# Optimization experiments

Measured on AMD Instinct MI355X. Metric: run time of the kernel, lower is better.

Reference implementation:

```python
import jax, jax.numpy as jnp
import numpy as np
from jax import lax

B, C_IN, H, W = 128, 3, 64, 64
HID = 128          # encoder hidden channels
D = 256            # embedding_dim
K = 1024           # codebook_size
COMMIT = 0.25      # commitment_cost


def conv(x, w, b, stride=2, pad=1):
    # x: NCHW, w: OIHW (torch Conv2d layout)
    y = lax.conv_general_dilated(x, w, (stride, stride), [(pad, pad), (pad, pad)],
                                 dimension_numbers=('NCHW', 'OIHW', 'NCHW'))
    return y + b[None, :, None, None]


def conv_t(x, w, b, stride=2, pad=1):
    # torch ConvTranspose2d: w is (in, out, kh, kw); equivalent to a conv with
    # lhs dilation = stride, flipped kernel, padding k-1-pad.
    k = w.shape[2]
    w_ = jnp.flip(w, (2, 3)).transpose(1, 0, 2, 3)  # -> (out, in, kh, kw)
    p = k - 1 - pad
    y = lax.conv_general_dilated(x, w_, (1, 1), [(p, p), (p, p)],
                                 lhs_dilation=(stride, stride),
                                 dimension_numbers=('NCHW', 'OIHW', 'NCHW'))
    return y + b[None, :, None, None]


def setup_inputs() -> dict:
    key = jax.random.key(0)
    ks = jax.random.split(key, 10)
    s = 0.05
    return {
        'x':        jax.random.normal(ks[0], (B, C_IN, H, W), jnp.float32),
        'enc_w1':   jax.random.normal(ks[1], (HID, C_IN, 4, 4), jnp.float32) * s,
        'enc_b1':   jnp.zeros((HID,), jnp.float32),
        'enc_w2':   jax.random.normal(ks[2], (D, HID, 4, 4), jnp.float32) * s,
        'enc_b2':   jnp.zeros((D,), jnp.float32),
        'dec_w1':   jax.random.normal(ks[3], (D, HID, 4, 4), jnp.float32) * s,   # ConvT: (in,out,kh,kw)
        'dec_b1':   jnp.zeros((HID,), jnp.float32),
        'dec_w2':   jax.random.normal(ks[4], (HID, C_IN, 4, 4), jnp.float32) * s,
        'dec_b2':   jnp.zeros((C_IN,), jnp.float32),
        'codebook': jax.random.normal(ks[5], (K, D), jnp.float32),  # embedding.weight.normal_()
    }


def vqvae_forward(x, enc_w1, enc_b1, enc_w2, enc_b2,
                  dec_w1, dec_b1, dec_w2, dec_b2, codebook):
    # ----- encoder -----
    h = jax.nn.relu(conv(x, enc_w1, enc_b1))          # (B, HID, 32, 32)
    e = conv(h, enc_w2, enc_b2)                        # (B, D, 16, 16)

    # ----- VectorQuantizerEMA.forward (eval mode, no mask) -----
    inputs = e.transpose(0, 2, 3, 1)                   # BCHW -> BHWC
    in_shape = inputs.shape
    flat = inputs.reshape(-1, D)                       # (N, D), N = B*16*16

    # squared L2 distances to every code: (N, K)
    dist = (jnp.sum(flat * flat, axis=1, keepdims=True)
            + jnp.sum(codebook * codebook, axis=1)
            - 2.0 * flat @ codebook.T)

    # max_one_hot(-distances) with straight-through gradients
    logits = -dist
    idx = jnp.argmax(logits, axis=-1)                  # (N,)
    oh = jax.nn.one_hot(idx, K, dtype=logits.dtype)
    flat_oh = oh + logits - lax.stop_gradient(logits)  # values == one-hot

    n_lat = in_shape[1] * in_shape[2]                  # H*W latents
    oh_encodings = flat_oh.reshape(in_shape[0], n_lat, K).transpose(0, 2, 1)  # (B, K, n)

    # quantize under no_grad (torch.no_grad block)
    quantized = lax.stop_gradient(flat_oh @ codebook).reshape(in_shape)

    e_latent_loss = jnp.mean((quantized - inputs) ** 2)
    loss = COMMIT * e_latent_loss

    # straight-through estimator
    quantized = inputs + lax.stop_gradient(quantized - inputs)

    avg_probs = jnp.mean(flat_oh, axis=0)
    perplexity = jnp.exp(-jnp.sum(avg_probs * jnp.log(avg_probs + 1e-10)))

    quantized_nchw = quantized.transpose(0, 3, 1, 2)   # BHWC -> BCHW

    # ----- decoder -----
    d1 = jax.nn.relu(conv_t(quantized_nchw, dec_w1, dec_b1))  # (B, HID, 32, 32)
    x_hat = conv_t(d1, dec_w2, dec_b2)                        # (B, 3, 64, 64)

    return x_hat, loss, perplexity, oh_encodings


def reference(x, enc_w1, enc_b1, enc_w2, enc_b2,
              dec_w1, dec_b1, dec_w2, dec_b2, codebook):
    return vqvae_forward(x, enc_w1, enc_b1, enc_w2, enc_b2,
                         dec_w1, dec_b1, dec_w2, dec_b2, codebook)
```

## Files before the change

kernel.cpp:

```cpp
#include <hip/hip_runtime.h>
#include <stdint.h>

#define NB   128
#define CIN  3
#define HID  128
#define DEM  256
#define KCB  1024
#define NLAT 32768

typedef __bf16 bf16x8 __attribute__((ext_vector_type(8)));
typedef _Float16 f16x8 __attribute__((ext_vector_type(8)));
typedef float  f32x4  __attribute__((ext_vector_type(4)));

__device__ inline unsigned short f2bf(float f) {
    unsigned u = __builtin_bit_cast(unsigned, f);
    u = (u + 0x7fff + ((u >> 16) & 1)) >> 16;
    return (unsigned short)u;
}

__global__ __launch_bounds__(256) void k_conv1(const float* __restrict__ x,
        const float* __restrict__ w, const float* __restrict__ bias,
        unsigned short* __restrict__ hA) {
    __shared__ float sx[3][66][66];
    const int b = blockIdx.y;
    const int ocg = blockIdx.x;
    const int oc0 = ocg * 16;
    const int tid = threadIdx.x;
    for (int i = tid; i < 3 * 66 * 66; i += 256) ((float*)sx)[i] = 0.f;
    __syncthreads();
    const float* xb = x + (size_t)b * (3 * 64 * 64);
    for (int i = tid; i < 3 * 64 * 64; i += 256) {
        int ic = i >> 12; int rem = i & 4095; int y = rem >> 6; int xx = rem & 63;
        sx[ic][y + 1][xx + 1] = xb[i];
    }
    __syncthreads();
    for (int j = 0; j < 4; ++j) {
        int pos = tid + j * 256;
        int oy = pos >> 5, ox = pos & 31;
        float acc[16];
        #pragma unroll
        for (int i = 0; i < 16; ++i) acc[i] = 0.f;
        int iy0 = 2 * oy;
        int ix0 = 2 * ox;
        for (int ic = 0; ic < 3; ++ic) {
            float p[16];
            #pragma unroll
            for (int ky = 0; ky < 4; ++ky)
                #pragma unroll
                for (int kx = 0; kx < 4; ++kx)
                    p[ky * 4 + kx] = sx[ic][iy0 + ky][ix0 + kx];
            #pragma unroll
            for (int oc = 0; oc < 16; ++oc) {
                const float* wp = w + ((oc0 + oc) * 3 + ic) * 16;
                float a = acc[oc];
                #pragma unroll
                for (int t = 0; t < 16; ++t) a = fmaf(p[t], wp[t], a);
                acc[oc] = a;
            }
        }
        unsigned short rec[32];
        #pragma unroll
        for (int oc = 0; oc < 16; ++oc) {
            float v = acc[oc] + bias[oc0 + oc];
            v = v > 0.f ? v : 0.f;
            _Float16 hh = (_Float16)v;
            float hf = (float)hh;
            _Float16 ll = (_Float16)((v - hf) * 2048.0f);
            rec[oc] = __builtin_bit_cast(unsigned short, hh);
            rec[16 + oc] = __builtin_bit_cast(unsigned short, ll);
        }
        uint4* dst = (uint4*)(hA + ((size_t)(b * 8 + ocg) * 1024 + pos) * 32);
        uint4* r4 = (uint4*)rec;
        dst[0] = r4[0]; dst[1] = r4[1]; dst[2] = r4[2]; dst[3] = r4[3];
    }
}

__global__ void k_packwf(const float* __restrict__ w, unsigned short* __restrict__ wpf) {
    int t = blockIdx.x * 256 + threadIdx.x;
    int oc = t >> 7, rest = t & 127;
    int c0 = rest >> 4, ci = rest & 15;
    const float* src = w + ((size_t)(oc * 128 + c0 * 16 + ci)) * 16;
    float tv[16];
    #pragma unroll
    for (int i = 0; i < 16; i += 4) {
        float4 v = *(const float4*)(src + i);
        tv[i] = v.x; tv[i + 1] = v.y; tv[i + 2] = v.z; tv[i + 3] = v.w;
    }
    int g = oc >> 4, lr = oc & 15;
    #pragma unroll
    for (int ks = 0; ks < 8; ++ks) {
        int ky = ks >> 1, kxp = ks & 1;
        #pragma unroll
        for (int kxh = 0; kxh < 2; ++kxh) {
            float v = tv[ky * 4 + 2 * kxp + kxh];
            _Float16 hh = (_Float16)v;
            float hf = (float)hh;
            _Float16 ll = (_Float16)((v - hf) * 2048.0f);
            int d = kxh * 16 + ci;
            int hi = d >> 3, el = d & 7;
            size_t base = ((((size_t)(c0 * 8 + ks) * 16 + g) * 2 + 0) * 4 + hi) * 128 + lr * 8 + el;
            wpf[base]       = __builtin_bit_cast(unsigned short, hh);
            wpf[base + 512] = __builtin_bit_cast(unsigned short, ll);
        }
    }
}

__global__ __launch_bounds__(512) void k_conv2_mfma(const unsigned short* __restrict__ hA,
        const unsigned short* __restrict__ wpf, const float* __restrict__ bias,
        float* __restrict__ e) {
    __shared__ __attribute__((aligned(16))) unsigned short As[577 * 40];
    const int tid = threadIdx.x;
    const int b = blockIdx.y;
    const int ocg = blockIdx.x >> 1, yh = blockIdx.x & 1;
    const int lane = tid & 63, wv = tid >> 6;
    const int wm = wv >> 2, wn = wv & 3;
    const int lr = lane & 15, hi = lane >> 4;

    if (tid < 40) As[576 * 40 + tid] = 0;

    f32x4 acc0[4][2], acc1[4][2];
    #pragma unroll
    for (int i = 0; i < 4; ++i)
        #pragma unroll
        for (int j = 0; j < 2; ++j) {
            acc0[i][j] = (f32x4){0.f, 0.f, 0.f, 0.f};
            acc1[i][j] = (f32x4){0.f, 0.f, 0.f, 0.f};
        }

    for (int c0 = 0; c0 < 8; ++c0) {
        __syncthreads();
        {
            const size_t cbase = (size_t)(b * 8 + c0) * 1024;
            for (int p = tid; p < 2304; p += 512) {
                int l = p >> 7, rem = p & 127;
                int ixs = rem >> 2, q = rem & 3;
                int iy = yh * 16 - 1 + l;
                uint4* dst = (uint4*)(As + (l * 32 + (ixs & 1) * 16 + (ixs >> 1)) * 40 + q * 8);
                if (iy >= 0 && iy < 32)
                    *dst = *(const uint4*)(hA + (cbase + iy * 32 + ixs) * 32 + q * 8);
                else
                    *dst = (uint4){0u, 0u, 0u, 0u};
            }
        }
        __syncthreads();
        #pragma unroll
        for (int ks = 0; ks < 8; ++ks) {
            const int ky = ks >> 1, kxp = ks & 1;
            f16x8 bh[2], bl[2];
            #pragma unroll
            for (int nf = 0; nf < 2; ++nf) {
                const unsigned short* bp = wpf
                    + ((((size_t)(c0 * 8 + ks) * 16 + (ocg * 8 + wn * 2 + nf)) * 2 + 0) * 4 + hi) * 128 + lr * 8;
                bh[nf] = *(const f16x8*)bp;
                bl[nf] = *(const f16x8*)(bp + 512);
            }
            const int o = 2 * kxp - 1 + (hi >> 1);
            const int ix = 2 * lr + o;
            const bool xv = (ix >= 0) && (ix < 32);
            const int sbase = (o & 1) * 16 + (ix >> 1);
            #pragma unroll
            for (int mf = 0; mf < 4; ++mf) {
                int l = 2 * (wm * 4 + mf) + ky;
                int slot = xv ? (l * 32 + sbase) : 576;
                const unsigned short* ap = As + slot * 40 + (hi & 1) * 8;
                f16x8 a0 = *(const f16x8*)ap;
                f16x8 a1 = *(const f16x8*)(ap + 16);
                #pragma unroll
                for (int nf = 0; nf < 2; ++nf) {
                    acc0[mf][nf] = __builtin_amdgcn_mfma_f32_16x16x32_f16(a0, bh[nf], acc0[mf][nf], 0, 0, 0);
                    acc1[mf][nf] = __builtin_amdgcn_mfma_f32_16x16x32_f16(a0, bl[nf], acc1[mf][nf], 0, 0, 0);
                    acc1[mf][nf] = __builtin_amdgcn_mfma_f32_16x16x32_f16(a1, bh[nf], acc1[mf][nf], 0, 0, 0);
                }
            }
        }
    }
    #pragma unroll
    for (int mf = 0; mf < 4; ++mf) {
        int oy = yh * 8 + wm * 4 + mf;
        #pragma unroll
        for (int nf = 0; nf < 2; ++nf) {
            int oc = ocg * 128 + wn * 32 + nf * 16 + lr;
            float bv = bias[oc];
            #pragma unroll
            for (int r = 0; r < 4; ++r) {
                int ox = hi * 4 + r;
                size_t erow = (size_t)b * 256 + (size_t)oy * 16 + ox;
                e[erow * 256 + oc] = acc0[mf][nf][r] + acc1[mf][nf][r] * (1.0f / 2048.0f) + bv;
            }
        }
    }
}

__global__ void k_cnorm(const float* __restrict__ cb, float* __restrict__ cn) {
    int k = blockIdx.x * 256 + threadIdx.x;
    const float* cp = cb + (size_t)k * 256;
    float s = 0.f;
    #pragma unroll 8
    for (int d = 0; d < 256; d += 4) {
        float4 v = *(const float4*)(cp + d);
        s = fmaf(v.x, v.x, s); s = fmaf(v.y, v.y, s);
        s = fmaf(v.z, v.z, s); s = fmaf(v.w, v.w, s);
    }
    cn[k] = s;
}

__global__ void k_packcbp(const float* __restrict__ cb, unsigned short* __restrict__ cbp) {
    int t = blockIdx.x * 256 + threadIdx.x;
    int c = t >> 8, d = t & 255;
    float v = cb[(size_t)c * 256 + d];
    _Float16 hh = (_Float16)v;
    float hf = (float)hh;
    _Float16 ll = (_Float16)((v - hf) * 2048.0f);
    int g = c >> 4, lr = c & 15;
    int kq = d >> 5, rem = d & 31, hi = rem >> 3, el = rem & 7;
    size_t b0 = ((((size_t)(g * 8 + kq) * 2 + 0) * 4 + hi) * 16 + lr) * 8 + el;
    size_t b1 = ((((size_t)(g * 8 + kq) * 2 + 1) * 4 + hi) * 16 + lr) * 8 + el;
    cbp[b0] = __builtin_bit_cast(unsigned short, hh);
    cbp[b1] = __builtin_bit_cast(unsigned short, ll);
}

__global__ __launch_bounds__(512) void k_vq_mfma(const float* __restrict__ e,
        const unsigned short* __restrict__ cbp, const float* __restrict__ cn,
        const float* __restrict__ cb,
        int* __restrict__ idx, int* __restrict__ counts, float* __restrict__ sse,
        float* __restrict__ oh) {
    __shared__ __attribute__((aligned(16))) unsigned short As[64 * 520];
    __shared__ float redS[8][64];
    __shared__ int   redI[8][64];
    __shared__ int   winner[64];
    __shared__ float sred[64];
    const int tid = threadIdx.x;
    const int lane = tid & 63;
    const int wv = tid >> 6;
    const int lr = lane & 15, hi = lane >> 4;
    const int row0 = blockIdx.x * 64;

    {
        int row = tid >> 3, seg = tid & 7;
        const float* src = e + (size_t)(row0 + row) * 256 + seg * 32;
        unsigned short hb[32], lb[32];
        #pragma unroll
        for (int i = 0; i < 32; i += 4) {
            float4 v = *(const float4*)(src + i);
            float vv[4] = {v.x, v.y, v.z, v.w};
            #pragma unroll
            for (int q = 0; q < 4; ++q) {
                _Float16 hh = (_Float16)vv[q];
                float hf = (float)hh;
                _Float16 ll = (_Float16)((vv[q] - hf) * 2048.0f);
                hb[i + q] = __builtin_bit_cast(unsigned short, hh);
                lb[i + q] = __builtin_bit_cast(unsigned short, ll);
            }
        }
        uint4* dh = (uint4*)(As + row * 520 + seg * 32);
        uint4* dl = (uint4*)(As + row * 520 + 256 + seg * 32);
        #pragma unroll
        for (int u = 0; u < 4; ++u) { dh[u] = ((uint4*)hb)[u]; dl[u] = ((uint4*)lb)[u]; }
    }
    __syncthreads();

    float best_s[4][4];
    int   best_i[4][4];
    #pragma unroll
    for (int a = 0; a < 4; ++a)
        #pragma unroll
        for (int r = 0; r < 4; ++r) { best_s[a][r] = 3.4e38f; best_i[a][r] = 0; }

    for (int ncg = 0; ncg < 4; ++ncg) {
        f32x4 acc0[4][2], acc1[4][2];
        #pragma unroll
        for (int i = 0; i < 4; ++i)
            #pragma unroll
            for (int j = 0; j < 2; ++j) {
                acc0[i][j] = (f32x4){0.f, 0.f, 0.f, 0.f};
                acc1[i][j] = (f32x4){0.f, 0.f, 0.f, 0.f};
            }
        const int gbase = ncg * 16 + wv * 2;
        #pragma unroll
        for (int kq = 0; kq < 8; ++kq) {
            f16x8 bh[2], bl[2];
            #pragma unroll
            for (int nf = 0; nf < 2; ++nf) {
                const unsigned short* bp = cbp
                    + (((size_t)((gbase + nf) * 8 + kq) * 2 + 0) * 4 + hi) * 128 + lr * 8;
                bh[nf] = *(const f16x8*)bp;
                bl[nf] = *(const f16x8*)(bp + 512);
            }
            #pragma unroll
            for (int mf = 0; mf < 4; ++mf) {
                const unsigned short* ap = As + (mf * 16 + lr) * 520 + kq * 32 + hi * 8;
                f16x8 a0 = *(const f16x8*)ap;
                f16x8 a1 = *(const f16x8*)(ap + 256);
                #pragma unroll
                for (int nf = 0; nf < 2; ++nf) {
                    acc0[mf][nf] = __builtin_amdgcn_mfma_f32_16x16x32_f16(a0, bh[nf], acc0[mf][nf], 0, 0, 0);
                    acc1[mf][nf] = __builtin_amdgcn_mfma_f32_16x16x32_f16(a0, bl[nf], acc1[mf][nf], 0, 0, 0);
                    acc1[mf][nf] = __builtin_amdgcn_mfma_f32_16x16x32_f16(a1, bh[nf], acc1[mf][nf], 0, 0, 0);
                }
            }
        }
        #pragma unroll
        for (int nf = 0; nf < 2; ++nf) {
            int code = (gbase + nf) * 16 + lr;
            float cnv = cn[code];
            #pragma unroll
            for (int mf = 0; mf < 4; ++mf)
                #pragma unroll
                for (int r = 0; r < 4; ++r) {
                    float dot = fmaf(acc1[mf][nf][r], (1.0f / 2048.0f), acc0[mf][nf][r]);
                    float s = fmaf(-2.0f, dot, cnv);
                    if (s < best_s[mf][r] || (s == best_s[mf][r] && code < best_i[mf][r])) {
                        best_s[mf][r] = s; best_i[mf][r] = code;
                    }
                }
        }
    }
    #pragma unroll
    for (int m = 1; m < 16; m <<= 1) {
        #pragma unroll
        for (int mf = 0; mf < 4; ++mf)
            #pragma unroll
            for (int r = 0; r < 4; ++r) {
                float os = __shfl_xor(best_s[mf][r], m, 64);
                int   oi = __shfl_xor(best_i[mf][r], m, 64);
                if (os < best_s[mf][r] || (os == best_s[mf][r] && oi < best_i[mf][r])) {
                    best_s[mf][r] = os; best_i[mf][r] = oi;
                }
            }
    }
    if (lr == 0) {
        #pragma unroll
        for (int mf = 0; mf < 4; ++mf)
            #pragma unroll
            for (int r = 0; r < 4; ++r) {
                int row = mf * 16 + hi * 4 + r;
                redS[wv][row] = best_s[mf][r];
                redI[wv][row] = best_i[mf][r];
            }
    }
    __syncthreads();
    if (tid < 64) {
        float bs = redS[0][tid]; int bi = redI[0][tid];
        for (int ww = 1; ww < 8; ++ww) {
            float s = redS[ww][tid]; int i2 = redI[ww][tid];
            if (s < bs || (s == bs && i2 < bi)) { bs = s; bi = i2; }
        }
        int rowg = row0 + tid;
        idx[rowg] = bi;
        atomicAdd(counts + bi, 1);
        int bimg = rowg >> 8, n = rowg & 255;
        oh[(size_t)bimg * (KCB * 256) + (size_t)bi * 256 + n] = 1.0f;
        winner[tid] = bi;
    }
    __syncthreads();
    {
        int row = tid >> 3, seg = tid & 7;
        int bi = winner[row];
        const float* cp = cb + (size_t)bi * 256 + seg * 32;
        const float* ep = e + (size_t)(row0 + row) * 256 + seg * 32;
        float s = 0.f;
        #pragma unroll
        for (int i = 0; i < 32; i += 4) {
            float4 a = *(const float4*)(cp + i);
            float4 b = *(const float4*)(ep + i);
            float d0 = a.x - b.x, d1 = a.y - b.y, d2 = a.z - b.z, d3 = a.w - b.w;
            s = fmaf(d0, d0, s); s = fmaf(d1, d1, s);
            s = fmaf(d2, d2, s); s = fmaf(d3, d3, s);
        }
        s += __shfl_down(s, 4, 64);
        s += __shfl_down(s, 2, 64);
        s += __shfl_down(s, 1, 64);
        if ((tid & 7) == 0) sred[row] = s;
    }
    __syncthreads();
    if (tid == 0) {
        float t = 0.f;
        for (int i = 0; i < 64; ++i) t += sred[i];
        atomicAdd(sse, t);
    }
}

__global__ void k_cb2bf(const float* __restrict__ cb, unsigned short* __restrict__ cbb) {
    int t = blockIdx.x * 256 + threadIdx.x;
    float4 v = *(const float4*)(cb + (size_t)t * 4);
    ushort4 o;
    o.x = f2bf(v.x); o.y = f2bf(v.y); o.z = f2bf(v.z); o.w = f2bf(v.w);
    *(ushort4*)(cbb + (size_t)t * 4) = o;
}

__global__ void k_packw(const float* __restrict__ w, unsigned short* __restrict__ wp) {
    int t = blockIdx.x * 256 + threadIdx.x;
    int ci = t >> 7, oc = t & 127;
    const float* src = w + ((size_t)ci * 128 + oc) * 16;
    float tv[16];
    #pragma unroll
    for (int i = 0; i < 16; i += 4) {
        float4 v = *(const float4*)(src + i);
        tv[i] = v.x; tv[i + 1] = v.y; tv[i + 2] = v.z; tv[i + 3] = v.w;
    }
    #pragma unroll
    for (int p = 0; p < 4; ++p) {
        int a = p >> 1, b2 = p & 1;
        #pragma unroll
        for (int tap = 0; tap < 4; ++tap) {
            int dy = tap >> 1, dx = tap & 1;
            float v = tv[((1 - a) + 2 * dy) * 4 + (1 - b2) + 2 * dx];
            wp[((((p * 4 + tap) * 128) + oc) << 8) + ci] = f2bf(v);
        }
    }
}

__global__ __launch_bounds__(512) void k_convt1_mfma(const int* __restrict__ idx,
        const unsigned short* __restrict__ cbb, const unsigned short* __restrict__ wp,
        const float* __restrict__ bias, float* __restrict__ d1) {
    __shared__ unsigned short As[257 * 72];
    __shared__ unsigned short Bs[128 * 72];
    __shared__ int sidx[256];
    const int tid = threadIdx.x;
    const int b  = blockIdx.y;
    const int p  = blockIdx.x;
    const int a  = p >> 1, bb2 = p & 1;
    if (tid < 256) sidx[tid] = idx[b * 256 + tid] * 256;
    if (tid < 72)  As[256 * 72 + tid] = 0;
    const int lane = tid & 63;
    const int w    = tid >> 6;
    const int wm = w >> 2, wn = w & 3;
    const int lr = lane & 15, hi = lane >> 4;
    const int koff = hi * 8;
    f32x4 acc[8][2];
    #pragma unroll
    for (int i = 0; i < 8; ++i)
        #pragma unroll
        for (int j = 0; j < 2; ++j) acc[i][j] = (f32x4){0.f, 0.f, 0.f, 0.f};

    for (int c0 = 0; c0 < 256; c0 += 64) {
        for (int tap = 0; tap < 4; ++tap) {
            __syncthreads();
            if (tap == 0) {
                int row = tid >> 1, half = tid & 1;
                const uint4* src = (const uint4*)(cbb + sidx[row] + c0 + half * 32);
                uint4 v0 = src[0], v1 = src[1], v2 = src[2], v3 = src[3];
                uint4* dst = (uint4*)(As + row * 72 + half * 32);
                dst[0] = v0; dst[1] = v1; dst[2] = v2; dst[3] = v3;
            }
            {
                int oc = tid >> 2, q = tid & 3;
                const uint4* src = (const uint4*)(wp + (((p * 4 + tap) * 128 + oc) << 8) + c0 + q * 16);
                uint4 v0 = src[0], v1 = src[1];
                uint4* dst = (uint4*)(Bs + oc * 72 + q * 16);
                dst[0] = v0; dst[1] = v1;
            }
            __syncthreads();
            const int dy = tap >> 1, dx = tap & 1;
            const int xo = lr + bb2 - dx;
            const bool xv = (xo >= 0) && (xo < 16);
            #pragma unroll
            for (int kk = 0; kk < 2; ++kk) {
                bf16x8 aF[8];
                #pragma unroll
                for (int i = 0; i < 8; ++i) {
                    int typ = wm * 8 + i + a - dy;
                    int row = (xv && typ >= 0 && typ < 16) ? typ * 16 + xo : 256;
                    aF[i] = *(const bf16x8*)(As + row * 72 + kk * 32 + koff);
                }
                #pragma unroll
                for (int j = 0; j < 2; ++j) {
                    bf16x8 bF = *(const bf16x8*)(Bs + ((wn * 2 + j) * 16 + lr) * 72 + kk * 32 + koff);
                    #pragma unroll
                    for (int i = 0; i < 8; ++i)
                        acc[i][j] = __builtin_amdgcn_mfma_f32_16x16x32_bf16(aF[i], bF, acc[i][j], 0, 0, 0);
                }
            }
        }
    }
    #pragma unroll
    for (int j = 0; j < 2; ++j) {
        int oc = (wn * 2 + j) * 16 + lr;
        float bv = bias[oc];
        #pragma unroll
        for (int i = 0; i < 8; ++i) {
            int mt = wm * 8 + i;
            int oy = 2 * mt + a;
            float* dp = d1 + (((size_t)b * 128 + oc) * 32 + oy) * 32 + bb2;
            #pragma unroll
            for (int r = 0; r < 4; ++r) {
                float v = acc[i][j][r] + bv;
                v = v > 0.f ? v : 0.f;
                dp[2 * (hi * 4 + r)] = v;
            }
        }
    }
}

__global__ __launch_bounds__(256) void k_convt2(const float* __restrict__ d1,
        const float* __restrict__ w, const float* __restrict__ bias,
        float* __restrict__ xhat) {
    __shared__ float sd[4][34][34];
    const int b = blockIdx.y;
    const int par = blockIdx.x;
    const int a = par >> 1, bb = par & 1;
    const int tid = threadIdx.x;
    const int ky0 = 1 - a, kx0 = 1 - bb;
    float acc[4][3];
    #pragma unroll
    for (int j = 0; j < 4; ++j)
        #pragma unroll
        for (int o = 0; o < 3; ++o) acc[j][o] = 0.f;
    for (int i = tid; i < 4 * 34 * 34; i += 256) ((float*)sd)[i] = 0.f;
    const float* db = d1 + (size_t)b * (128 * 1024);
    for (int c0 = 0; c0 < 128; c0 += 4) {
        __syncthreads();
        for (int i = tid; i < 4096; i += 256) {
            int ci = i >> 10, rem = i & 1023, y = rem >> 5, xx = rem & 31;
            sd[ci][y + 1][xx + 1] = db[(c0 + ci) * 1024 + rem];
        }
        __syncthreads();
        #pragma unroll
        for (int j = 0; j < 4; ++j) {
            int pos = tid + j * 256;
            int my = pos >> 5, mx = pos & 31;
            int iy0 = my + a, ix0 = mx + bb;
            #pragma unroll
            for (int ci = 0; ci < 4; ++ci) {
                float q00 = sd[ci][iy0 + 1][ix0 + 1];
                float q01 = sd[ci][iy0 + 1][ix0];
                float q10 = sd[ci][iy0][ix0 + 1];
                float q11 = sd[ci][iy0][ix0];
                const float* wp = w + (size_t)(c0 + ci) * 3 * 16;
                #pragma unroll
                for (int o = 0; o < 3; ++o) {
                    const float* wq = wp + o * 16;
                    float aa = acc[j][o];
                    aa = fmaf(q00, wq[ky0 * 4 + kx0], aa);
                    aa = fmaf(q01, wq[ky0 * 4 + kx0 + 2], aa);
                    aa = fmaf(q10, wq[(ky0 + 2) * 4 + kx0], aa);
                    aa = fmaf(q11, wq[(ky0 + 2) * 4 + kx0 + 2], aa);
                    acc[j][o] = aa;
                }
            }
        }
    }
    #pragma unroll
    for (int j = 0; j < 4; ++j) {
        int pos = tid + j * 256;
        int my = pos >> 5, mx = pos & 31;
        int oy = 2 * my + a, ox = 2 * mx + bb;
        #pragma unroll
        for (int o = 0; o < 3; ++o)
            xhat[((size_t)b * 3 + o) * 4096 + oy * 64 + ox] = acc[j][o] + bias[o];
    }
}

__global__ void k_final(const int* __restrict__ counts, const float* __restrict__ sse,
                        float* __restrict__ out_loss, float* __restrict__ out_perp) {
    __shared__ float red[256];
    int tid = threadIdx.x;
    float s = 0.f;
    for (int k = tid; k < 1024; k += 256) {
        float p = (float)counts[k] * (1.f / 32768.f);
        s += p * logf(p + 1e-10f);
    }
    red[tid] = s;
    __syncthreads();
    for (int st = 128; st > 0; st >>= 1) {
        if (tid < st) red[tid] += red[tid + st];
        __syncthreads();
    }
    if (tid == 0) {
        *out_perp = expf(-red[0]);
        *out_loss = 0.25f * (*sse) / 8388608.0f;
    }
}

extern "C" void kernel_launch(void* const* d_in, const int* in_sizes, int n_in,
                              void* d_out, int out_size, void* d_ws, size_t ws_size,
                              hipStream_t stream) {
    const float* x   = (const float*)d_in[0];
    const float* ew1 = (const float*)d_in[1];
    const float* eb1 = (const float*)d_in[2];
    const float* ew2 = (const float*)d_in[3];
    const float* eb2 = (const float*)d_in[4];
    const float* dw1 = (const float*)d_in[5];
    const float* db1 = (const float*)d_in[6];
    const float* dw2 = (const float*)d_in[7];
    const float* db2 = (const float*)d_in[8];
    const float* cb  = (const float*)d_in[9];

    float* out  = (float*)d_out;
    float* xhat = out;
    float* loss = out + 1572864;
    float* perp = out + 1572865;
    float* oh   = out + 1572866;

    char* ws = (char*)d_ws;
    unsigned short* hA = (unsigned short*)ws;
    float* e      = (float*)(ws + (size_t)64 * 1024 * 1024);
    int*   idx    = (int*)(ws + (size_t)96 * 1024 * 1024);
    int*   counts = idx + NLAT;
    float* sse    = (float*)(counts + KCB);
    float* cn     = sse + 1;
    unsigned short* cbp = (unsigned short*)ws;
    float* d1     = (float*)ws;
    unsigned short* cbb = (unsigned short*)e;
    unsigned short* wpk = (unsigned short*)(ws + (size_t)65 * 1024 * 1024);
    unsigned short* wpf = (unsigned short*)(((uintptr_t)oh + 15) & ~(uintptr_t)15);

    hipMemsetAsync(oh, 0, (size_t)33554432 * 4, stream);
    hipMemsetAsync(counts, 0, KCB * 4 + 4, stream);

    k_cnorm<<<4, 256, 0, stream>>>(cb, cn);
    k_packwf<<<128, 256, 0, stream>>>(ew2, wpf);
    k_conv1<<<dim3(8, 128), 256, 0, stream>>>(x, ew1, eb1, hA);
    k_conv2_mfma<<<dim3(4, 128), 512, 0, stream>>>(hA, wpf, eb2, e);
    hipMemsetAsync(oh, 0, 2 * 1024 * 1024 + 64, stream);
    k_packcbp<<<1024, 256, 0, stream>>>(cb, cbp);
    k_vq_mfma<<<512, 512, 0, stream>>>(e, cbp, cn, cb, idx, counts, sse, oh);
    k_cb2bf<<<256, 256, 0, stream>>>(cb, cbb);
    k_packw<<<128, 256, 0, stream>>>(dw1, wpk);
    k_convt1_mfma<<<dim3(4, 128), 512, 0, stream>>>(idx, cbb, wpk, db1, d1);
    k_convt2<<<dim3(4, 128), 256, 0, stream>>>(d1, dw2, db2, xhat);
    k_final<<<1, 256, 0, stream>>>(counts, sse, loss, perp);
}
```

Measured before the change: 671.4 us.

## Enlarge VQ block tile to 128 rows to halve codebook reloads

The VQ distance kernel now processes 128 latent rows per block instead of 64, so each codebook fragment loaded from global memory is reused across twice as many rows, and the grid is halved to 256 blocks. Each wave now owns one code group per phase over 8 phases instead of two groups over 4. LDS usage roughly doubles to about 133 KB and the accumulator count stays the same. The risk is lower occupancy, and with fewer blocks than CUs the machine may be underfilled.

```diff
diff --git a/kernel.cpp b/kernel.cpp
--- a/kernel.cpp
+++ b/kernel.cpp
@@ -219,24 +219,25 @@
     cbp[b1] = __builtin_bit_cast(unsigned short, ll);
 }
 
-__global__ __launch_bounds__(512) void k_vq_mfma(const float* __restrict__ e,
+__global__ __launch_bounds__(512, 2) void k_vq_mfma(const float* __restrict__ e,
         const unsigned short* __restrict__ cbp, const float* __restrict__ cn,
         const float* __restrict__ cb,
         int* __restrict__ idx, int* __restrict__ counts, float* __restrict__ sse,
         float* __restrict__ oh) {
-    __shared__ __attribute__((aligned(16))) unsigned short As[64 * 520];
-    __shared__ float redS[8][64];
-    __shared__ int   redI[8][64];
-    __shared__ int   winner[64];
-    __shared__ float sred[64];
+    __shared__ __attribute__((aligned(16))) unsigned short As[128 * 520];
+    __shared__ float redS[8][128];
+    __shared__ int   redI[8][128];
+    __shared__ int   winner[128];
+    __shared__ float sred[128];
     const int tid = threadIdx.x;
     const int lane = tid & 63;
     const int wv = tid >> 6;
     const int lr = lane & 15, hi = lane >> 4;
-    const int row0 = blockIdx.x * 64;
-
-    {
-        int row = tid >> 3, seg = tid & 7;
+    const int row0 = blockIdx.x * 128;
+
+    #pragma unroll
+    for (int rr = 0; rr < 2; ++rr) {
+        int row = rr * 64 + (tid >> 3), seg = tid & 7;
         const float* src = e + (size_t)(row0 + row) * 256 + seg * 32;
         unsigned short hb[32], lb[32];
         #pragma unroll
@@ -259,87 +260,90 @@
     }
     __syncthreads();
 
-    float best_s[4][4];
-    int   best_i[4][4];
-    #pragma unroll
-    for (int a = 0; a < 4; ++a)
-        #pragma unroll
-        for (int r = 0; r < 4; ++r) { best_s[a][r] = 3.4e38f; best_i[a][r] = 0; }
-
-    for (int ncg = 0; ncg < 4; ++ncg) {
-        f32x4 acc0[4][2], acc1[4][2];
-        #pragma unroll
-        for (int i = 0; i < 4; ++i)
-            #pragma unroll
-            for (int j = 0; j < 2; ++j) {
-                acc0[i][j] = (f32x4){0.f, 0.f, 0.f, 0.f};
-                acc1[i][j] = (f32x4){0.f, 0.f, 0.f, 0.f};
-            }
-        const int gbase = ncg * 16 + wv * 2;
+    float best_s[2][4][4];
+    int   best_i[2][4][4];
+    #pragma unroll
+    for (int rh = 0; rh < 2; ++rh)
+        #pragma unroll
+        for (int a = 0; a < 4; ++a)
+            #pragma unroll
+            for (int r = 0; r < 4; ++r) { best_s[rh][a][r] = 3.4e38f; best_i[rh][a][r] = 0; }
+
+    for (int ph = 0; ph < 8; ++ph) {
+        const int gidx = ph * 8 + wv;
+        f32x4 acc0[2][4], acc1[2][4];
+        #pragma unroll
+        for (int rh = 0; rh < 2; ++rh)
+            #pragma unroll
+            for (int i = 0; i < 4; ++i) {
+                acc0[rh][i] = (f32x4){0.f, 0.f, 0.f, 0.f};
+                acc1[rh][i] = (f32x4){0.f, 0.f, 0.f, 0.f};
+            }
         #pragma unroll
         for (int kq = 0; kq < 8; ++kq) {
-            f16x8 bh[2], bl[2];
-            #pragma unroll
-            for (int nf = 0; nf < 2; ++nf) {
-                const unsigned short* bp = cbp
-                    + (((size_t)((gbase + nf) * 8 + kq) * 2 + 0) * 4 + hi) * 128 + lr * 8;
-                bh[nf] = *(const f16x8*)bp;
-                bl[nf] = *(const f16x8*)(bp + 512);
-            }
-            #pragma unroll
-            for (int mf = 0; mf < 4; ++mf) {
-                const unsigned short* ap = As + (mf * 16 + lr) * 520 + kq * 32 + hi * 8;
-                f16x8 a0 = *(const f16x8*)ap;
-                f16x8 a1 = *(const f16x8*)(ap + 256);
-                #pragma unroll
-                for (int nf = 0; nf < 2; ++nf) {
-                    acc0[mf][nf] = __builtin_amdgcn_mfma_f32_16x16x32_f16(a0, bh[nf], acc0[mf][nf], 0, 0, 0);
-                    acc1[mf][nf] = __builtin_amdgcn_mfma_f32_16x16x32_f16(a0, bl[nf], acc1[mf][nf], 0, 0, 0);
-                    acc1[mf][nf] = __builtin_amdgcn_mfma_f32_16x16x32_f16(a1, bh[nf], acc1[mf][nf], 0, 0, 0);
+            const unsigned short* bp = cbp
+                + (((size_t)(gidx * 8 + kq) * 2 + 0) * 4 + hi) * 128 + lr * 8;
+            f16x8 bh = *(const f16x8*)bp;
+            f16x8 bl = *(const f16x8*)(bp + 512);
+            #pragma unroll
+            for (int rh = 0; rh < 2; ++rh) {
+                #pragma unroll
+                for (int mf = 0; mf < 4; ++mf) {
+                    const unsigned short* ap = As + (rh * 64 + mf * 16 + lr) * 520 + kq * 32 + hi * 8;
+                    f16x8 a0 = *(const f16x8*)ap;
+                    f16x8 a1 = *(const f16x8*)(ap + 256);
+                    acc0[rh][mf] = __builtin_amdgcn_mfma_f32_16x16x32_f16(a0, bh, acc0[rh][mf], 0, 0, 0);
+                    acc1[rh][mf] = __builtin_amdgcn_mfma_f32_16x16x32_f16(a0, bl, acc1[rh][mf], 0, 0, 0);
+                    acc1[rh][mf] = __builtin_amdgcn_mfma_f32_16x16x32_f16(a1, bh, acc1[rh][mf], 0, 0, 0);
                 }
             }
         }
-        #pragma unroll
-        for (int nf = 0; nf < 2; ++nf) {
-            int code = (gbase + nf) * 16 + lr;
+        {
+            int code = gidx * 16 + lr;
             float cnv = cn[code];
             #pragma unroll
+            for (int rh = 0; rh < 2; ++rh)
+                #pragma unroll
+                for (int mf = 0; mf < 4; ++mf)
+                    #pragma unroll
+                    for (int r = 0; r < 4; ++r) {
+                        float dot = fmaf(acc1[rh][mf][r], (1.0f / 2048.0f), acc0[rh][mf][r]);
+                        float s = fmaf(-2.0f, dot, cnv);
+                        if (s < best_s[rh][mf][r] || (s == best_s[rh][mf][r] && code < best_i[rh][mf][r])) {
+                            best_s[rh][mf][r] = s; best_i[rh][mf][r] = code;
+                        }
+                    }
+        }
+    }
+    #pragma unroll
+    for (int m = 1; m < 16; m <<= 1) {
+        #pragma unroll
+        for (int rh = 0; rh < 2; ++rh)
+            #pragma unroll
             for (int mf = 0; mf < 4; ++mf)
                 #pragma unroll
                 for (int r = 0; r < 4; ++r) {
-                    float dot = fmaf(acc1[mf][nf][r], (1.0f / 2048.0f), acc0[mf][nf][r]);
-                    float s = fmaf(-2.0f, dot, cnv);
-                    if (s < best_s[mf][r] || (s == best_s[mf][r] && code < best_i[mf][r])) {
-                        best_s[mf][r] = s; best_i[mf][r] = code;
+                    float os = __shfl_xor(best_s[rh][mf][r], m, 64);
+                    int   oi = __shfl_xor(best_i[rh][mf][r], m, 64);
+                    if (os < best_s[rh][mf][r] || (os == best_s[rh][mf][r] && oi < best_i[rh][mf][r])) {
+                        best_s[rh][mf][r] = os; best_i[rh][mf][r] = oi;
                     }
                 }
-        }
-    }
-    #pragma unroll
-    for (int m = 1; m < 16; m <<= 1) {
-        #pragma unroll
-        for (int mf = 0; mf < 4; ++mf)
-            #pragma unroll
-            for (int r = 0; r < 4; ++r) {
-                float os = __shfl_xor(best_s[mf][r], m, 64);
-                int   oi = __shfl_xor(best_i[mf][r], m, 64);
-                if (os < best_s[mf][r] || (os == best_s[mf][r] && oi < best_i[mf][r])) {
-                    best_s[mf][r] = os; best_i[mf][r] = oi;
+    }
+    if (lr == 0) {
+        #pragma unroll
+        for (int rh = 0; rh < 2; ++rh)
+            #pragma unroll
+            for (int mf = 0; mf < 4; ++mf)
+                #pragma unroll
+                for (int r = 0; r < 4; ++r) {
+                    int row = rh * 64 + mf * 16 + hi * 4 + r;
+                    redS[wv][row] = best_s[rh][mf][r];
+                    redI[wv][row] = best_i[rh][mf][r];
                 }
-            }
-    }
-    if (lr == 0) {
-        #pragma unroll
-        for (int mf = 0; mf < 4; ++mf)
-            #pragma unroll
-            for (int r = 0; r < 4; ++r) {
-                int row = mf * 16 + hi * 4 + r;
-                redS[wv][row] = best_s[mf][r];
-                redI[wv][row] = best_i[mf][r];
-            }
     }
     __syncthreads();
-    if (tid < 64) {
+    if (tid < 128) {
         float bs = redS[0][tid]; int bi = redI[0][tid];
         for (int ww = 1; ww < 8; ++ww) {
             float s = redS[ww][tid]; int i2 = redI[ww][tid];
@@ -354,28 +358,27 @@
     }
     __syncthreads();
     {
-        int row = tid >> 3, seg = tid & 7;
+        int row = tid >> 2, seg = tid & 3;
         int bi = winner[row];
-        const float* cp = cb + (size_t)bi * 256 + seg * 32;
-        const float* ep = e + (size_t)(row0 + row) * 256 + seg * 32;
+        const float* cp = cb + (size_t)bi * 256 + seg * 64;
+        const float* ep = e + (size_t)(row0 + row) * 256 + seg * 64;
         float s = 0.f;
         #pragma unroll
-        for (int i = 0; i < 32; i += 4) {
+        for (int i = 0; i < 64; i += 4) {
             float4 a = *(const float4*)(cp + i);
             float4 b = *(const float4*)(ep + i);
             float d0 = a.x - b.x, d1 = a.y - b.y, d2 = a.z - b.z, d3 = a.w - b.w;
             s = fmaf(d0, d0, s); s = fmaf(d1, d1, s);
             s = fmaf(d2, d2, s); s = fmaf(d3, d3, s);
         }
-        s += __shfl_down(s, 4, 64);
         s += __shfl_down(s, 2, 64);
         s += __shfl_down(s, 1, 64);
-        if ((tid & 7) == 0) sred[row] = s;
+        if ((tid & 3) == 0) sred[row] = s;
     }
     __syncthreads();
     if (tid == 0) {
         float t = 0.f;
-        for (int i = 0; i < 64; ++i) t += sred[i];
+        for (int i = 0; i < 128; ++i) t += sred[i];
         atomicAdd(sse, t);
     }
 }
@@ -614,7 +617,7 @@
     k_conv2_mfma<<<dim3(4, 128), 512, 0, stream>>>(hA, wpf, eb2, e);
     hipMemsetAsync(oh, 0, 2 * 1024 * 1024 + 64, stream);
     k_packcbp<<<1024, 256, 0, stream>>>(cb, cbp);
-    k_vq_mfma<<<512, 512, 0, stream>>>(e, cbp, cn, cb, idx, counts, sse, oh);
+    k_vq_mfma<<<256, 512, 0, stream>>>(e, cbp, cn, cb, idx, counts, sse, oh);
     k_cb2bf<<<256, 256, 0, stream>>>(cb, cbb);
     k_packw<<<128, 256, 0, stream>>>(dw1, wpk);
     k_convt1_mfma<<<dim3(4, 128), 512, 0, stream>>>(idx, cbb, wpk, db1, d1);
```

Result: slower. 949.6 us (+41.4%).

## Run second transposed conv on bf16 MFMA with NHWC bf16 intermediate

Applied to the files above, without the earlier changes.

The first transposed conv now writes its output as bf16 in NHWC layout instead of fp32 NCHW, and the scalar FMA second transposed conv is replaced by an MFMA kernel. That kernel pads the 3 output channels to 16 and tiles four parity taps over channel groups, using a new pre-packed weight buffer. The aim is to halve the intermediate's memory traffic and move the 128-channel reduction onto matrix cores. The cost is bf16 rounding of the intermediate activation, some wasted MFMA lanes from the padding, and scattered bf16 stores in the first kernel.

```diff
diff --git a/kernel.cpp b/kernel.cpp
--- a/kernel.cpp
+++ b/kernel.cpp
@@ -410,9 +410,26 @@
     }
 }
 
+__global__ void k_packw2t(const float* __restrict__ w, unsigned short* __restrict__ wt) {
+    int t = blockIdx.x * 256 + threadIdx.x;
+    int el = t & 7, lr = (t >> 3) & 15, hi = (t >> 7) & 3;
+    int cig = (t >> 9) & 3, tp = (t >> 11) & 3, p = (t >> 13) & 3;
+    int ci = cig * 32 + hi * 8 + el;
+    int a = p >> 1, bb = p & 1;
+    int ky0 = 1 - a, kx0 = 1 - bb;
+    int wtap;
+    if (tp == 0) wtap = ky0 * 4 + kx0;
+    else if (tp == 1) wtap = ky0 * 4 + kx0 + 2;
+    else if (tp == 2) wtap = (ky0 + 2) * 4 + kx0;
+    else wtap = (ky0 + 2) * 4 + kx0 + 2;
+    unsigned short v = 0;
+    if (lr < 3) v = f2bf(w[((size_t)ci * 3 + lr) * 16 + wtap]);
+    wt[t] = v;
+}
+
 __global__ __launch_bounds__(512) void k_convt1_mfma(const int* __restrict__ idx,
         const unsigned short* __restrict__ cbb, const unsigned short* __restrict__ wp,
-        const float* __restrict__ bias, float* __restrict__ d1) {
+        const float* __restrict__ bias, unsigned short* __restrict__ d1b) {
     __shared__ unsigned short As[257 * 72];
     __shared__ unsigned short Bs[128 * 72];
     __shared__ int sidx[256];
@@ -481,73 +498,71 @@
         for (int i = 0; i < 8; ++i) {
             int mt = wm * 8 + i;
             int oy = 2 * mt + a;
-            float* dp = d1 + (((size_t)b * 128 + oc) * 32 + oy) * 32 + bb2;
             #pragma unroll
             for (int r = 0; r < 4; ++r) {
+                int ox = bb2 + 2 * (hi * 4 + r);
                 float v = acc[i][j][r] + bv;
                 v = v > 0.f ? v : 0.f;
-                dp[2 * (hi * 4 + r)] = v;
-            }
-        }
-    }
-}
-
-__global__ __launch_bounds__(256) void k_convt2(const float* __restrict__ d1,
-        const float* __restrict__ w, const float* __restrict__ bias,
+                d1b[(((size_t)b * 32 + oy) * 32 + ox) * 128 + oc] = f2bf(v);
+            }
+        }
+    }
+}
+
+__global__ __launch_bounds__(512) void k_convt2_mfma(const unsigned short* __restrict__ d1b,
+        const unsigned short* __restrict__ wt, const float* __restrict__ bias,
         float* __restrict__ xhat) {
-    __shared__ float sd[4][34][34];
+    __shared__ __attribute__((aligned(16))) unsigned short sd[18 * 34 * 32];
+    const int tid = threadIdx.x;
     const int b = blockIdx.y;
-    const int par = blockIdx.x;
-    const int a = par >> 1, bb = par & 1;
-    const int tid = threadIdx.x;
-    const int ky0 = 1 - a, kx0 = 1 - bb;
-    float acc[4][3];
-    #pragma unroll
-    for (int j = 0; j < 4; ++j)
-        #pragma unroll
-        for (int o = 0; o < 3; ++o) acc[j][o] = 0.f;
-    for (int i = tid; i < 4 * 34 * 34; i += 256) ((float*)sd)[i] = 0.f;
-    const float* db = d1 + (size_t)b * (128 * 1024);
-    for (int c0 = 0; c0 < 128; c0 += 4) {
+    const int p = blockIdx.x >> 1, yh = blockIdx.x & 1;
+    const int a = p >> 1, bb = p & 1;
+    const int lane = tid & 63, wv = tid >> 6;
+    const int lr = lane & 15, hi = lane >> 4;
+
+    f32x4 acc[4];
+    #pragma unroll
+    for (int i = 0; i < 4; ++i) acc[i] = (f32x4){0.f, 0.f, 0.f, 0.f};
+
+    for (int cig = 0; cig < 4; ++cig) {
         __syncthreads();
-        for (int i = tid; i < 4096; i += 256) {
-            int ci = i >> 10, rem = i & 1023, y = rem >> 5, xx = rem & 31;
-            sd[ci][y + 1][xx + 1] = db[(c0 + ci) * 1024 + rem];
+        for (int q4 = tid; q4 < 2448; q4 += 512) {
+            int l = q4 / 136, rem = q4 % 136, xx = rem >> 2, q = rem & 3;
+            int iy = yh * 16 - 1 + l, ixx = xx - 1;
+            uint4* dst = (uint4*)(sd + (l * 34 + xx) * 32 + q * 8);
+            if (iy >= 0 && iy < 32 && ixx >= 0 && ixx < 32)
+                *dst = *(const uint4*)(d1b + (((size_t)b * 32 + iy) * 32 + ixx) * 128 + cig * 32 + q * 8);
+            else
+                *dst = (uint4){0u, 0u, 0u, 0u};
         }
         __syncthreads();
         #pragma unroll
-        for (int j = 0; j < 4; ++j) {
-            int pos = tid + j * 256;
-            int my = pos >> 5, mx = pos & 31;
-            int iy0 = my + a, ix0 = mx + bb;
-            #pragma unroll
-            for (int ci = 0; ci < 4; ++ci) {
-                float q00 = sd[ci][iy0 + 1][ix0 + 1];
-                float q01 = sd[ci][iy0 + 1][ix0];
-                float q10 = sd[ci][iy0][ix0 + 1];
-                float q11 = sd[ci][iy0][ix0];
-                const float* wp = w + (size_t)(c0 + ci) * 3 * 16;
-                #pragma unroll
-                for (int o = 0; o < 3; ++o) {
-                    const float* wq = wp + o * 16;
-                    float aa = acc[j][o];
-                    aa = fmaf(q00, wq[ky0 * 4 + kx0], aa);
-                    aa = fmaf(q01, wq[ky0 * 4 + kx0 + 2], aa);
-                    aa = fmaf(q10, wq[(ky0 + 2) * 4 + kx0], aa);
-                    aa = fmaf(q11, wq[(ky0 + 2) * 4 + kx0 + 2], aa);
-                    acc[j][o] = aa;
-                }
-            }
-        }
-    }
-    #pragma unroll
-    for (int j = 0; j < 4; ++j) {
-        int pos = tid + j * 256;
-        int my = pos >> 5, mx = pos & 31;
-        int oy = 2 * my + a, ox = 2 * mx + bb;
-        #pragma unroll
-        for (int o = 0; o < 3; ++o)
-            xhat[((size_t)b * 3 + o) * 4096 + oy * 64 + ox] = acc[j][o] + bias[o];
+        for (int tp = 0; tp < 4; ++tp) {
+            const unsigned short* bp = wt + ((((p * 4 + tp) * 4 + cig) * 4 + hi) * 16 + lr) * 8;
+            bf16x8 bF = *(const bf16x8*)bp;
+            #pragma unroll
+            for (int mf = 0; mf < 4; ++mf) {
+                int pos = wv * 64 + mf * 16 + lr;
+                int myl = pos >> 5, mx = pos & 31;
+                int l = myl + a + (tp < 2 ? 1 : 0);
+                int xx = mx + bb + ((tp & 1) ? 0 : 1);
+                bf16x8 aF = *(const bf16x8*)(sd + (l * 34 + xx) * 32 + hi * 8);
+                acc[mf] = __builtin_amdgcn_mfma_f32_16x16x32_bf16(aF, bF, acc[mf], 0, 0, 0);
+            }
+        }
+    }
+    if (lr < 3) {
+        float bv = bias[lr];
+        #pragma unroll
+        for (int mf = 0; mf < 4; ++mf) {
+            #pragma unroll
+            for (int r = 0; r < 4; ++r) {
+                int pos = wv * 64 + mf * 16 + hi * 4 + r;
+                int oy = 2 * (yh * 16 + (pos >> 5)) + a;
+                int ox = 2 * (pos & 31) + bb;
+                xhat[(((size_t)b * 3 + lr) * 64 + oy) * 64 + ox] = acc[mf][r] + bv;
+            }
+        }
     }
 }
 
@@ -600,9 +615,10 @@
     float* sse    = (float*)(counts + KCB);
     float* cn     = sse + 1;
     unsigned short* cbp = (unsigned short*)ws;
-    float* d1     = (float*)ws;
+    unsigned short* d1b = (unsigned short*)ws;
     unsigned short* cbb = (unsigned short*)e;
     unsigned short* wpk = (unsigned short*)(ws + (size_t)65 * 1024 * 1024);
+    unsigned short* wt  = (unsigned short*)(ws + (size_t)67 * 1024 * 1024);
     unsigned short* wpf = (unsigned short*)(((uintptr_t)oh + 15) & ~(uintptr_t)15);
 
     hipMemsetAsync(oh, 0, (size_t)33554432 * 4, stream);
@@ -617,7 +633,8 @@
     k_vq_mfma<<<512, 512, 0, stream>>>(e, cbp, cn, cb, idx, counts, sse, oh);
     k_cb2bf<<<256, 256, 0, stream>>>(cb, cbb);
     k_packw<<<128, 256, 0, stream>>>(dw1, wpk);
-    k_convt1_mfma<<<dim3(4, 128), 512, 0, stream>>>(idx, cbb, wpk, db1, d1);
-    k_convt2<<<dim3(4, 128), 256, 0, stream>>>(d1, dw2, db2, xhat);
+    k_packw2t<<<128, 256, 0, stream>>>(dw2, wt);
+    k_convt1_mfma<<<dim3(4, 128), 512, 0, stream>>>(idx, cbb, wpk, db1, d1b);
+    k_convt2_mfma<<<dim3(8, 128), 512, 0, stream>>>(d1b, wt, db2, xhat);
     k_final<<<1, 256, 0, stream>>>(counts, sse, loss, perp);
 }
```

Result: faster. 584.0 us (-13.0%).
